# Optimization experiments

Hardware: AMD Instinct MI355X
Metric: run time of the kernel (lower is better)

## Reference

```python
import jax, jax.numpy as jnp
import numpy as np

N = 20000   # nodes
E = 320000  # edges
H = 128     # hidden_dim
L = 4       # num_layers
OUT = 64    # output_dim
XD = 16     # node_input_dim


def setup_inputs() -> dict:
    key = jax.random.key(0)
    ks = jax.random.split(key, 32)

    def w(k, shape):
        fan_in = shape[-2] if len(shape) >= 2 else shape[-1]
        return (jax.random.normal(k, shape, jnp.float32) / np.sqrt(fan_in)).astype(jnp.float32)

    inp = {
        'y': jax.random.normal(ks[0], (N, 6), jnp.float32),
        'x': jax.random.normal(ks[1], (N, XD), jnp.float32),
        'edge_attr': jax.random.normal(ks[2], (E, 8), jnp.float32),
        'edge_index': jax.random.randint(ks[3], (2, E), 0, N),
        'W_node': w(ks[4], (XD, H)),        'b_node': jnp.zeros((H,), jnp.float32),
        'W_eemb': w(ks[5], (5, H - 3)),     'b_eemb': jnp.zeros((H - 3,), jnp.float32),
        'W_msg': w(ks[6], (L, 3 * H + 1, H)), 'b_msg': jnp.zeros((L, H), jnp.float32),
        'W_upd': w(ks[7], (L, 2 * H, H)),     'b_upd': jnp.zeros((L, H), jnp.float32),
        'ln_g': jnp.ones((L, H), jnp.float32), 'ln_b': jnp.zeros((L, H), jnp.float32),
        'W_eu': w(ks[8], (L, 3 * H, H)),      'b_eu': jnp.zeros((L, H), jnp.float32),
        'W_out': w(ks[9], (H, OUT)),          'b_out': jnp.zeros((OUT,), jnp.float32),
        'Wh1': w(ks[10], (OUT, OUT // 2)),    'bh1': jnp.zeros((OUT // 2,), jnp.float32),
        'Wh2': w(ks[11], (OUT // 2, 1)),      'bh2': jnp.zeros((1,), jnp.float32),
    }
    return inp


def _drift(y, x, edge_attr, W_node, b_node, W_eemb, b_eemb, W_msg, b_msg,
           W_upd, b_upd, ln_g, ln_b, W_eu, b_eu, W_out, b_out,
           Wh1, bh1, Wh2, bh2, edge_index):
    src, dst = edge_index[0], edge_index[1]
    q, p = jnp.split(y, 2, axis=-1)  # each [N,3]

    def potential(q):
        pos = q
        h = x @ W_node + b_node                                    # [N,H]
        e = jnp.concatenate([edge_attr[:, :3],
                             edge_attr[:, 3:] @ W_eemb + b_eemb], -1)  # [E,H]
        for l in range(L):
            rel = pos[dst] - pos[src]                              # [E,3]
            dist = jnp.sqrt(jnp.sum(rel * rel, -1, keepdims=True) + 1e-8)
            m_in = jnp.concatenate([h[src], h[dst], e, dist], -1)  # [E,3H+1]
            m = jax.nn.silu(m_in @ W_msg[l] + b_msg[l])            # [E,H]
            agg = jax.ops.segment_sum(m, dst, num_segments=N)      # [N,H]
            u = jnp.concatenate([h, agg], -1) @ W_upd[l] + b_upd[l]
            mu = jnp.mean(u, -1, keepdims=True)
            var = jnp.var(u, -1, keepdims=True)
            u = (u - mu) / jnp.sqrt(var + 1e-5) * ln_g[l] + ln_b[l]
            h = h + jax.nn.silu(u)
            e = e + jax.nn.silu(jnp.concatenate([h[src], h[dst], e], -1) @ W_eu[l] + b_eu[l])
        f = h @ W_out + b_out                                      # [N,OUT]
        v = jax.nn.silu(f @ Wh1 + bh1) @ Wh2 + bh2                 # [N,1]
        return jnp.sum(v)

    grad_q = jax.grad(potential)(q)      # dH/dq
    # dH/dp = p (kinetic 0.5*sum(p*p)); drift = (dH/dp, -dH/dq)
    return jnp.concatenate([p, -grad_q], axis=-1)


def reference(y, x, edge_attr, edge_index, W_node, b_node, W_eemb, b_eemb,
              W_msg, b_msg, W_upd, b_upd, ln_g, ln_b, W_eu, b_eu,
              W_out, b_out, Wh1, bh1, Wh2, bh2):
    return _drift(y, x, edge_attr, W_node, b_node, W_eemb, b_eemb, W_msg, b_msg,
                  W_upd, b_upd, ln_g, ln_b, W_eu, b_eu, W_out, b_out,
                  Wh1, bh1, Wh2, bh2, edge_index)
```

## Files before the change

### kernel.cpp

```cpp
#include <hip/hip_runtime.h>
#include <hip/hip_bf16.h>

#define NN 20000
#define NE 320000
#define H  128
#define NL 4

typedef unsigned int uint;
typedef unsigned short u16;
typedef short s8v __attribute__((ext_vector_type(8)));
typedef float fx4 __attribute__((ext_vector_type(4)));

static constexpr size_t NNH = (size_t)NN*H;
static constexpr size_t NEH = (size_t)NE*H;

static constexpr size_t OFF_H5    = 0;
static constexpr size_t OFF_UPRE  = OFF_H5    + 5*NNH*2;
static constexpr size_t OFF_LNST  = OFF_UPRE  + 4*NNH*2;
static constexpr size_t OFF_T     = OFF_LNST  + (size_t)4*NN*2*4;
static constexpr size_t OFF_E     = OFF_T     + 4*NNH*2;
static constexpr size_t OFF_DE    = OFF_E     + NEH*2;
static constexpr size_t OFF_AGG   = OFF_DE    + NEH*2;
static constexpr size_t OFF_DH    = OFF_AGG   + NNH*4;
static constexpr size_t OFF_DIST  = OFF_DH    + NNH*4;
static constexpr size_t OFF_DDIST = OFF_DIST  + (size_t)NE*4;
static constexpr size_t OFF_DPOS  = OFF_DDIST + (size_t)NE*4;
static constexpr size_t OFF_WMT   = OFF_DPOS  + (size_t)NN*3*4;
static constexpr size_t OFF_WET   = OFF_WMT   + (size_t)NL*128*388*4;
static constexpr size_t OFF_WUT   = OFF_WET   + (size_t)NL*128*384*4;
static constexpr size_t OFF_PD    = OFF_WUT   + (size_t)NL*128*256*4;
static constexpr size_t OFF_PS    = OFF_PD    + (size_t)NE*4;
static constexpr size_t OFF_CURD  = OFF_PS    + (size_t)NE*4;
static constexpr size_t OFF_CURS  = OFF_CURD  + (size_t)NN*4;
static constexpr size_t OFF_WMP   = OFF_CURS  + (size_t)NN*4;
static constexpr size_t OFF_WEP   = OFF_WMP   + (size_t)NL*49152*2;
static constexpr size_t OFF_WMTP  = OFF_WEP   + (size_t)NL*49152*2;
static constexpr size_t OFF_WETP  = OFF_WMTP  + (size_t)NL*49152*2;
static constexpr size_t WS_NEED   = OFF_WETP  + (size_t)NL*49152*2;

__device__ __forceinline__ float sigm(float x){ return 1.f/(1.f+__expf(-x)); }
__device__ __forceinline__ float siluf(float x){ return x*sigm(x); }
__device__ __forceinline__ float dsilu(float x){ float s=sigm(x); return s*(1.f + x*(1.f-s)); }
__device__ __forceinline__ u16 f2bf(float x){
  uint u = __float_as_uint(x);
  uint r = (u + 0x7fffu + ((u>>16)&1u)) >> 16;
  return (u16)r;
}
__device__ __forceinline__ float bf2f(u16 v){ return __uint_as_float(((uint)v)<<16); }
__device__ __forceinline__ uint pack2(float a, float b){ return (uint)f2bf(a) | ((uint)f2bf(b)<<16); }
__device__ __forceinline__ void ld_bf8(const u16* p, float* v){
  uint4 q = *(const uint4*)p;
  v[0]=__uint_as_float(q.x<<16); v[1]=__uint_as_float(q.x&0xffff0000u);
  v[2]=__uint_as_float(q.y<<16); v[3]=__uint_as_float(q.y&0xffff0000u);
  v[4]=__uint_as_float(q.z<<16); v[5]=__uint_as_float(q.z&0xffff0000u);
  v[6]=__uint_as_float(q.w<<16); v[7]=__uint_as_float(q.w&0xffff0000u);
}
__device__ __forceinline__ void st_bf8(u16* p, const float* v){
  uint4 o;
  o.x = pack2(v[0],v[1]); o.y = pack2(v[2],v[3]);
  o.z = pack2(v[4],v[5]); o.w = pack2(v[6],v[7]);
  *(uint4*)p = o;
}

__device__ __forceinline__ float2 blockSum2_128(float a, float b, float* sb){
  #pragma unroll
  for (int off=32; off>0; off>>=1){ a += __shfl_down(a, off); b += __shfl_down(b, off); }
  int t = threadIdx.x;
  if ((t&63)==0){ sb[(t>>6)*2+0]=a; sb[(t>>6)*2+1]=b; }
  __syncthreads();
  float2 r; r.x = sb[0]+sb[2]; r.y = sb[1]+sb[3];
  __syncthreads();
  return r;
}

__device__ __forceinline__ void seg_walk136(const u16* Cst, const int* keys, float* buf, int t){
  int c = t & 127, half = t >> 7;
  int i0 = half*64, i1 = i0 + 64;
  float acc = 0.f; int k = keys[i0];
  #pragma unroll 4
  for (int i=i0; i<i1; i++){
    int ki = keys[i];
    if (ki != k){ atomicAdd(&buf[(size_t)k*H + c], acc); acc = 0.f; k = ki; }
    acc += bf2f(Cst[(size_t)i*136 + c]);
  }
  atomicAdd(&buf[(size_t)k*H + c], acc);
}

__global__ void diag_k(float* out, float v){ out[0] = v; }

__global__ void hist_k(const int* __restrict__ ei, int* __restrict__ curs, int* __restrict__ curd){
  int e = blockIdx.x*256 + threadIdx.x;
  if (e >= NE) return;
  atomicAdd(&curs[ei[e]], 1);
  atomicAdd(&curd[ei[NE+e]], 1);
}

__global__ __launch_bounds__(256) void scan_k(int* __restrict__ curd, int* __restrict__ curs){
  __shared__ int ps[256];
  const int t = threadIdx.x;
  const int CH = (NN + 255)/256;
  for (int a=0; a<2; a++){
    int* p = a ? curs : curd;
    int lo = t*CH, hi = lo+CH < NN ? lo+CH : NN;
    int sum = 0;
    for (int i=lo; i<hi; i++) sum += p[i];
    ps[t] = sum;
    __syncthreads();
    #pragma unroll
    for (int off=1; off<256; off<<=1){
      int v = (t>=off) ? ps[t-off] : 0;
      __syncthreads();
      ps[t] += v;
      __syncthreads();
    }
    int run = (t==0) ? 0 : ps[t-1];
    for (int i=lo; i<hi; i++){ int v = p[i]; p[i] = run; run += v; }
    __syncthreads();
  }
}

__global__ void fill_k(const int* __restrict__ ei, int* __restrict__ curs, int* __restrict__ curd,
                       int* __restrict__ perm_s, int* __restrict__ perm_d){
  int e = blockIdx.x*256 + threadIdx.x;
  if (e >= NE) return;
  perm_s[atomicAdd(&curs[ei[e]], 1)] = e;
  perm_d[atomicAdd(&curd[ei[NE+e]], 1)] = e;
}

__global__ void transpose_w(const float* __restrict__ Wm, const float* __restrict__ We,
                            const float* __restrict__ Wu,
                            float* __restrict__ WmT, float* __restrict__ WeT,
                            float* __restrict__ WuT){
  int idx = blockIdx.x*blockDim.x + threadIdx.x;
  int stride = gridDim.x*blockDim.x;
  for (int i=idx; i<NL*128*388; i+=stride){
    int l = i/(128*388), r = i - l*128*388, k = r/388, j = r - k*388;
    WmT[i] = (j<385) ? Wm[((size_t)l*385 + j)*H + k] : 0.f;
  }
  for (int i=idx; i<NL*128*384; i+=stride){
    int l = i/(128*384), r = i - l*128*384, k = r/384, j = r - k*384;
    WeT[i] = We[((size_t)l*384 + j)*H + k];
  }
  for (int i=idx; i<NL*128*256; i+=stride){
    int l = i/(128*256), r = i - l*128*256, k = r/256, j = r - k*256;
    WuT[i] = Wu[((size_t)l*256 + j)*H + k];
  }
}

__global__ __launch_bounds__(64) void pack_k(const float* __restrict__ src, u16* __restrict__ dst,
                      int KS, int NC, int ld, size_t sStride, size_t dStride){
  int b = blockIdx.x;
  int l = b/(KS*NC); int r = b - l*KS*NC; int ks = r/NC; int ct = r - ks*NC;
  int lane = threadIdx.x;
  #pragma unroll
  for (int j=0;j<8;j++){
    int k = ks*32 + (lane>>4)*8 + j;
    int c = ct*16 + (lane&15);
    dst[l*dStride + ((size_t)(ks*NC+ct)*64 + lane)*8 + j] =
        f2bf(src[l*sStride + (size_t)k*ld + c]);
  }
}

__global__ __launch_bounds__(128) void node_emb(const float* __restrict__ x,
                                                const float* __restrict__ Wn,
                                                const float* __restrict__ bn,
                                                u16* __restrict__ h){
  __shared__ float xs[16];
  int n = blockIdx.x, c = threadIdx.x;
  if (c < 16) xs[c] = x[(size_t)n*16 + c];
  __syncthreads();
  float s = bn[c];
  #pragma unroll
  for (int k=0;k<16;k++) s = fmaf(xs[k], Wn[k*H + c], s);
  h[(size_t)n*H + c] = f2bf(s);
}

__global__ __launch_bounds__(256) void edge_emb(const float* __restrict__ ea,
                                                const float* __restrict__ We5,
                                                const float* __restrict__ be,
                                                u16* __restrict__ ebuf){
  int e = blockIdx.x*2 + (threadIdx.x>>7);
  int c = threadIdx.x & 127;
  const float* row = ea + (size_t)e*8;
  float v;
  if (c < 3) v = row[c];
  else {
    int j = c-3;
    float s = be[j];
    #pragma unroll
    for (int k=0;k<5;k++) s = fmaf(row[3+k], We5[k*125 + j], s);
    v = s;
  }
  ebuf[(size_t)e*H + c] = f2bf(v);
}

__global__ void rel_dist(const float* __restrict__ y, const int* __restrict__ ei,
                         float* __restrict__ dist){
  int e = blockIdx.x*256 + threadIdx.x;
  if (e >= NE) return;
  int s = ei[e], d = ei[NE+e];
  float rx = y[(size_t)d*6+0] - y[(size_t)s*6+0];
  float ry = y[(size_t)d*6+1] - y[(size_t)s*6+1];
  float rz = y[(size_t)d*6+2] - y[(size_t)s*6+2];
  dist[e] = sqrtf(rx*rx + ry*ry + rz*rz + 1e-8f);
}

#define PHASE1_MFMA(ACC)                                                          \
  _Pragma("unroll 1")                                                             \
  for (int s=0; s<12; s++){                                                       \
    s8v av0, av1;                                                                 \
    {                                                                             \
      int k = s*32 + l4*8;                                                        \
      int row0 = wid*32 + li, row1 = row0 + 16;                                   \
      const u16 *p0, *p1;                                                         \
      if (k < 128){ p0 = hb + (size_t)sidx[row0]*H + k;                           \
                    p1 = hb + (size_t)sidx[row1]*H + k; }                         \
      else if (k < 256){ p0 = hb + (size_t)didx[row0]*H + (k-128);                \
                         p1 = hb + (size_t)didx[row1]*H + (k-128); }              \
      else { p0 = eb + (size_t)eidl[row0]*H + (k-256);                            \
             p1 = eb + (size_t)eidl[row1]*H + (k-256); }                          \
      av0 = *(const s8v*)p0; av1 = *(const s8v*)p1;                               \
    }                                                                             \
    _Pragma("unroll")                                                             \
    for (int ct=0; ct<8; ct++){                                                   \
      s8v bv = *(const s8v*)&WP[((size_t)(s*8+ct)*64 + lane)*8];                  \
      ACC[0][ct] = __builtin_amdgcn_mfma_f32_16x16x32_bf16(av0, bv, ACC[0][ct], 0,0,0); \
      ACC[1][ct] = __builtin_amdgcn_mfma_f32_16x16x32_bf16(av1, bv, ACC[1][ct], 0,0,0); \
    }                                                                             \
  }

template<int MODE>
__global__ __launch_bounds__(256) void efwd(
    const u16* __restrict__ hb, u16* __restrict__ eb,
    const float* __restrict__ dist, const int* __restrict__ ei,
    const int* __restrict__ perm,
    const float* __restrict__ Wf, const float* __restrict__ bias,
    const u16* __restrict__ WP,
    float* __restrict__ agg, float* __restrict__ Tf)
{
  __shared__ __align__(16) u16 Als[128*136];
  __shared__ int eidl[128], sidx[128], didx[128];
  const int t = threadIdx.x;
  const int e0 = blockIdx.x * 128;
  if (t < 128){
    int eid = perm ? perm[e0+t] : (e0+t);
    eidl[t] = eid; sidx[t] = ei[eid]; didx[t] = ei[NE+eid];
  }
  __syncthreads();
  const int lane = t&63, wid = t>>6, l4 = lane>>4, li = lane&15;

  fx4 acc[2][8];
  #pragma unroll
  for (int i=0;i<2;i++){
    #pragma unroll
    for (int j=0;j<8;j++) acc[i][j] = (fx4){0.f,0.f,0.f,0.f};
  }
  PHASE1_MFMA(acc)

  float dv[2][4];
  if (MODE==0){
    #pragma unroll
    for (int rt=0;rt<2;rt++){
      #pragma unroll
      for (int reg=0;reg<4;reg++) dv[rt][reg] = dist[eidl[wid*32+rt*16+l4*4+reg]];
    }
  }
  #pragma unroll
  for (int ct=0; ct<8; ct++){
    int c = ct*16 + li;
    float bi = bias[c];
    float wd = (MODE==0) ? Wf[(size_t)384*H + c] : 0.f;
    #pragma unroll
    for (int rt=0;rt<2;rt++){
      #pragma unroll
      for (int reg=0;reg<4;reg++)
        acc[rt][ct][reg] += bi + ((MODE==0) ? dv[rt][reg]*wd : 0.f);
    }
  }

  if (MODE==0){
    __syncthreads();
    #pragma unroll
    for (int rt=0;rt<2;rt++){
      #pragma unroll
      for (int reg=0;reg<4;reg++){
        int brow = wid*32+rt*16+l4*4+reg;
        #pragma unroll
        for (int ct=0;ct<8;ct++)
          Als[(size_t)brow*136 + ct*16+li] = f2bf(siluf(acc[rt][ct][reg]));
      }
    }
    __syncthreads();
    seg_walk136(Als, didx, agg, t);
    __syncthreads();
    #pragma unroll
    for (int rt=0;rt<2;rt++){
      #pragma unroll
      for (int reg=0;reg<4;reg++){
        int brow = wid*32+rt*16+l4*4+reg;
        #pragma unroll
        for (int ct=0;ct<8;ct++)
          Als[(size_t)brow*136 + ct*16+li] = f2bf(dsilu(acc[rt][ct][reg]));
      }
    }
    __syncthreads();
    seg_walk136(Als, didx, Tf, t);
  } else {
    __syncthreads();
    #pragma unroll
    for (int rt=0;rt<2;rt++){
      #pragma unroll
      for (int reg=0;reg<4;reg++){
        int brow = wid*32+rt*16+l4*4+reg;
        #pragma unroll
        for (int ct=0;ct<8;ct++)
          Als[(size_t)brow*136 + ct*16+li] = f2bf(siluf(acc[rt][ct][reg]));
      }
    }
    __syncthreads();
    int row = t>>1, coff = (t&1)*64;
    u16* dst = eb + (size_t)eidl[row]*H + coff;
    #pragma unroll
    for (int i=0;i<8;i++){
      float a[8], b[8];
      ld_bf8(&Als[(size_t)row*136 + coff + i*8], a);
      ld_bf8(&dst[i*8], b);
      #pragma unroll
      for (int j=0;j<8;j++) b[j] += a[j];
      st_bf8(&dst[i*8], b);
    }
  }
}

template<int MODE>
__global__ __launch_bounds__(256) void ebwd(
    const u16* __restrict__ hb, const u16* __restrict__ eb,
    const float* __restrict__ dist, const int* __restrict__ ei,
    const int* __restrict__ perm,
    const float* __restrict__ Wf, const float* __restrict__ bias,
    const float* __restrict__ mulf, const float* __restrict__ WTf,
    const u16* __restrict__ WP, const u16* __restrict__ WTP,
    float* __restrict__ dh, u16* __restrict__ de, float* __restrict__ ddist)
{
  __shared__ __align__(16) u16 Als[128*136];
  __shared__ int eidl[128], sidx[128], didx[128];
  const int t = threadIdx.x;
  const int e0 = blockIdx.x * 128;
  if (t < 128){
    int eid = perm[e0+t];
    eidl[t] = eid; sidx[t] = ei[eid]; didx[t] = ei[NE+eid];
  }
  __syncthreads();
  const int lane = t&63, wid = t>>6, l4 = lane>>4, li = lane&15;

  fx4 acc[2][8];
  #pragma unroll
  for (int i=0;i<2;i++){
    #pragma unroll
    for (int j=0;j<8;j++) acc[i][j] = (fx4){0.f,0.f,0.f,0.f};
  }
  PHASE1_MFMA(acc)

  float dv[2][4];
  if (MODE==0){
    #pragma unroll
    for (int rt=0;rt<2;rt++){
      #pragma unroll
      for (int reg=0;reg<4;reg++) dv[rt][reg] = dist[eidl[wid*32+rt*16+l4*4+reg]];
    }
  }
  #pragma unroll
  for (int ct=0; ct<8; ct++){
    int c = ct*16 + li;
    float bi = bias[c];
    float wd = (MODE==0) ? Wf[(size_t)384*H + c] : 0.f;
    #pragma unroll
    for (int rt=0;rt<2;rt++){
      #pragma unroll
      for (int reg=0;reg<4;reg++)
        acc[rt][ct][reg] += bi + ((MODE==0) ? dv[rt][reg]*wd : 0.f);
    }
  }

  if (MODE==1){
    {
      int row = t>>1, coff = (t&1)*64;
      const u16* src = de + (size_t)eidl[row]*H + coff;
      #pragma unroll
      for (int i=0;i<8;i++)
        *(uint4*)&Als[(size_t)row*136 + coff + i*8] = *(const uint4*)&src[i*8];
    }
    __syncthreads();
  }
  #pragma unroll
  for (int rt=0;rt<2;rt++){
    #pragma unroll
    for (int reg=0;reg<4;reg++){
      int brow = wid*32+rt*16+l4*4+reg;
      #pragma unroll
      for (int ct=0;ct<8;ct++){
        int c = ct*16+li;
        float m;
        if (MODE==0) m = mulf[(size_t)didx[brow]*H + c];
        else         m = bf2f(Als[(size_t)brow*136 + c]);
        acc[rt][ct][reg] = m * dsilu(acc[rt][ct][reg]);
      }
    }
  }

  if (MODE==0){
    float wdT[8];
    #pragma unroll
    for (int ct=0;ct<8;ct++) wdT[ct] = WTf[(size_t)(ct*16+li)*388 + 384];
    #pragma unroll
    for (int rt=0;rt<2;rt++){
      #pragma unroll
      for (int reg=0;reg<4;reg++){
        float pd = 0.f;
        #pragma unroll
        for (int ct=0;ct<8;ct++) pd = fmaf(acc[rt][ct][reg], wdT[ct], pd);
        pd += __shfl_xor(pd, 1);
        pd += __shfl_xor(pd, 2);
        pd += __shfl_xor(pd, 4);
        pd += __shfl_xor(pd, 8);
        if (li == 0) ddist[eidl[wid*32+rt*16+l4*4+reg]] += pd;
      }
    }
  }

  __syncthreads();
  #pragma unroll
  for (int rt=0;rt<2;rt++){
    #pragma unroll
    for (int reg=0;reg<4;reg++){
      int brow = wid*32+rt*16+l4*4+reg;
      #pragma unroll
      for (int ct=0;ct<8;ct++)
        Als[(size_t)brow*136 + ct*16+li] = f2bf(acc[rt][ct][reg]);
    }
  }
  __syncthreads();

  s8v afr[2][4];
  #pragma unroll
  for (int rt=0;rt<2;rt++){
    int row = wid*32 + rt*16 + li;
    #pragma unroll
    for (int ks=0;ks<4;ks++)
      afr[rt][ks] = *(const s8v*)&Als[(size_t)row*136 + ks*32 + l4*8];
  }

  const int njc = (MODE==0) ? 2 : 3;
  const int jcl[3] = {2, (MODE==0)?0:1, 0};
  #pragma unroll 1
  for (int ji=0; ji<njc; ji++){
    const int jc = jcl[ji];
    #pragma unroll
    for (int i=0;i<2;i++){
      #pragma unroll
      for (int j=0;j<8;j++) acc[i][j] = (fx4){0.f,0.f,0.f,0.f};
    }
    #pragma unroll
    for (int ks=0;ks<4;ks++){
      #pragma unroll
      for (int ct=0;ct<8;ct++){
        s8v bv = *(const s8v*)&WTP[((size_t)(ks*24 + jc*8 + ct)*64 + lane)*8];
        acc[0][ct] = __builtin_amdgcn_mfma_f32_16x16x32_bf16(afr[0][ks], bv, acc[0][ct], 0,0,0);
        acc[1][ct] = __builtin_amdgcn_mfma_f32_16x16x32_bf16(afr[1][ks], bv, acc[1][ct], 0,0,0);
      }
    }
    if (jc == 1){
      #pragma unroll
      for (int rt=0;rt<2;rt++){
        #pragma unroll
        for (int reg=0;reg<4;reg++){
          int dn = didx[wid*32+rt*16+l4*4+reg];
          #pragma unroll
          for (int ct=0;ct<8;ct++)
            atomicAdd(&dh[(size_t)dn*H + ct*16+li], acc[rt][ct][reg]);
        }
      }
    } else {
      __syncthreads();
      #pragma unroll
      for (int rt=0;rt<2;rt++){
        #pragma unroll
        for (int reg=0;reg<4;reg++){
          int brow = wid*32+rt*16+l4*4+reg;
          #pragma unroll
          for (int ct=0;ct<8;ct++)
            Als[(size_t)brow*136 + ct*16+li] = f2bf(acc[rt][ct][reg]);
        }
      }
      __syncthreads();
      if (jc == 2){
        int row = t>>1, coff = (t&1)*64;
        u16* dst = de + (size_t)eidl[row]*H + coff;
        #pragma unroll
        for (int i=0;i<8;i++){
          float a[8], b[8];
          ld_bf8(&Als[(size_t)row*136 + coff + i*8], a);
          ld_bf8(&dst[i*8], b);
          #pragma unroll
          for (int j=0;j<8;j++) b[j] += a[j];
          st_bf8(&dst[i*8], b);
        }
      } else {
        seg_walk136(Als, sidx, dh, t);
      }
    }
  }
}

__global__ __launch_bounds__(128) void upd_fwd(
    const u16* __restrict__ hin, const float* __restrict__ agg,
    const float* __restrict__ Wu, const float* __restrict__ bu,
    const float* __restrict__ g, const float* __restrict__ bln,
    u16* __restrict__ upre, float* __restrict__ lnst, u16* __restrict__ hout,
    u16* __restrict__ T, float* __restrict__ Tf)
{
  __shared__ float ha[8][256];
  __shared__ float sb[4];
  const int n0 = blockIdx.x*8, c = threadIdx.x;
  #pragma unroll
  for (int n=0;n<8;n++){
    ha[n][c]     = bf2f(hin[(size_t)(n0+n)*H + c]);
    ha[n][128+c] = agg[(size_t)(n0+n)*H + c];
  }
  __syncthreads();
  float s[8];
  float bv = bu[c];
  #pragma unroll
  for (int n=0;n<8;n++) s[n] = bv;
  #pragma unroll 2
  for (int k=0;k<256;k++){
    float w = Wu[(size_t)k*H + c];
    #pragma unroll
    for (int n=0;n<8;n++) s[n] = fmaf(ha[n][k], w, s[n]);
  }
  float gc = g[c], bc = bln[c];
  #pragma unroll 1
  for (int n=0;n<8;n++){
    int nn = n0+n;
    upre[(size_t)nn*H + c] = f2bf(s[n]);
    float2 ms = blockSum2_128(s[n], s[n]*s[n], sb);
    float mu = ms.x*(1.f/128.f);
    float var = ms.y*(1.f/128.f) - mu*mu;
    float rstd = rsqrtf(var + 1e-5f);
    if (c == 0){ lnst[(size_t)nn*2+0] = mu; lnst[(size_t)nn*2+1] = rstd; }
    float uh = (s[n] - mu)*rstd;
    float un = uh*gc + bc;
    hout[(size_t)nn*H + c] = f2bf(ha[n][c] + siluf(un));
    size_t idx = (size_t)nn*H + c;
    T[idx] = f2bf(Tf[idx]);
    Tf[idx] = 0.f;
  }
}

__global__ __launch_bounds__(128) void final_fused(
    const u16* __restrict__ h, const float* __restrict__ Wo, const float* __restrict__ bo,
    const float* __restrict__ Wh1, const float* __restrict__ bh1v,
    const float* __restrict__ Wh2, float* __restrict__ dh)
{
  __shared__ float sh[8][128], sf[8][64], sdz[8][32], sdf[8][64];
  const int n0 = blockIdx.x*8, c = threadIdx.x;
  #pragma unroll
  for (int n=0;n<8;n++) sh[n][c] = bf2f(h[(size_t)(n0+n)*H + c]);
  __syncthreads();
  if (c < 64){
    float s[8]; float bv = bo[c];
    #pragma unroll
    for (int n=0;n<8;n++) s[n] = bv;
    #pragma unroll 2
    for (int k=0;k<128;k++){
      float w = Wo[(size_t)k*64 + c];
      #pragma unroll
      for (int n=0;n<8;n++) s[n] = fmaf(sh[n][k], w, s[n]);
    }
    #pragma unroll
    for (int n=0;n<8;n++) sf[n][c] = s[n];
  }
  __syncthreads();
  if (c < 32){
    float s[8]; float bv = bh1v[c];
    #pragma unroll
    for (int n=0;n<8;n++) s[n] = bv;
    #pragma unroll 2
    for (int j=0;j<64;j++){
      float w = Wh1[(size_t)j*32 + c];
      #pragma unroll
      for (int n=0;n<8;n++) s[n] = fmaf(sf[n][j], w, s[n]);
    }
    float w2 = Wh2[c];
    #pragma unroll
    for (int n=0;n<8;n++) sdz[n][c] = w2*dsilu(s[n]);
  }
  __syncthreads();
  if (c < 64){
    float s[8];
    #pragma unroll
    for (int n=0;n<8;n++) s[n] = 0.f;
    #pragma unroll 2
    for (int k=0;k<32;k++){
      float w = Wh1[(size_t)c*32 + k];
      #pragma unroll
      for (int n=0;n<8;n++) s[n] = fmaf(sdz[n][k], w, s[n]);
    }
    #pragma unroll
    for (int n=0;n<8;n++) sdf[n][c] = s[n];
  }
  __syncthreads();
  {
    float s[8];
    #pragma unroll
    for (int n=0;n<8;n++) s[n] = 0.f;
    #pragma unroll 2
    for (int j=0;j<64;j++){
      float w = Wo[(size_t)c*64 + j];
      #pragma unroll
      for (int n=0;n<8;n++) s[n] = fmaf(sdf[n][j], w, s[n]);
    }
    #pragma unroll
    for (int n=0;n<8;n++) dh[(size_t)(n0+n)*H + c] = s[n];
  }
}

__global__ __launch_bounds__(128) void upd_bwd(
    float* __restrict__ dh, float* __restrict__ dagg,
    const u16* __restrict__ upre, const float* __restrict__ lnst,
    const float* __restrict__ WuT, const u16* __restrict__ T,
    const float* __restrict__ WmT,
    const float* __restrict__ g, const float* __restrict__ bln)
{
  __shared__ float sh[8][128];
  __shared__ float qs[8][128];
  __shared__ float sb[4];
  const int n0 = blockIdx.x*8, c = threadIdx.x;
  const float gc = g[c], bc = bln[c];
  float dhv[8];
  #pragma unroll 1
  for (int n=0;n<8;n++){
    int nn = n0+n;
    float up   = bf2f(upre[(size_t)nn*H + c]);
    float mu   = lnst[(size_t)nn*2+0];
    float rstd = lnst[(size_t)nn*2+1];
    float uh = (up - mu)*rstd;
    float un = uh*gc + bc;
    dhv[n] = dh[(size_t)nn*H + c];
    float dun = dhv[n] * dsilu(un);
    float duh = dun * gc;
    float2 m12 = blockSum2_128(duh, duh*uh, sb);
    sh[n][c] = (duh - m12.x*(1.f/128.f) - uh*(m12.y*(1.f/128.f)))*rstd;
  }
  __syncthreads();
  float s0[8], s1[8];
  #pragma unroll
  for (int n=0;n<8;n++){ s0[n]=0.f; s1[n]=0.f; }
  #pragma unroll 2
  for (int k=0;k<128;k++){
    float w0 = WuT[(size_t)k*256 + c];
    float w1 = WuT[(size_t)k*256 + 128 + c];
    #pragma unroll
    for (int n=0;n<8;n++){
      float d = sh[n][k];
      s0[n] = fmaf(d, w0, s0[n]);
      s1[n] = fmaf(d, w1, s1[n]);
    }
  }
  #pragma unroll
  for (int n=0;n<8;n++){
    int nn = n0+n;
    dagg[(size_t)nn*H + c] = s1[n];
    qs[n][c] = s1[n] * bf2f(T[(size_t)nn*H + c]);
  }
  __syncthreads();
  float a2[8];
  #pragma unroll
  for (int n=0;n<8;n++) a2[n] = 0.f;
  #pragma unroll 2
  for (int k=0;k<128;k++){
    float w = WmT[(size_t)k*388 + 128 + c];
    #pragma unroll
    for (int n=0;n<8;n++) a2[n] = fmaf(qs[n][k], w, a2[n]);
  }
  #pragma unroll
  for (int n=0;n<8;n++) dh[(size_t)(n0+n)*H + c] = dhv[n] + s0[n] + a2[n];
}

__global__ void rel_bwd(const float* __restrict__ y, const float* __restrict__ dist,
                        const float* __restrict__ ddist, const int* __restrict__ ei,
                        float* __restrict__ dpos){
  int e = blockIdx.x*256 + threadIdx.x;
  if (e >= NE) return;
  int s = ei[e], d = ei[NE+e];
  float gsc = ddist[e]/dist[e];
  #pragma unroll
  for (int i=0;i<3;i++){
    float dr = gsc*(y[(size_t)d*6+i] - y[(size_t)s*6+i]);
    atomicAdd(&dpos[(size_t)d*3+i],  dr);
    atomicAdd(&dpos[(size_t)s*3+i], -dr);
  }
}

__global__ void out_k(const float* __restrict__ y, const float* __restrict__ dpos,
                      float* __restrict__ out){
  int n = blockIdx.x*256 + threadIdx.x;
  if (n >= NN) return;
  #pragma unroll
  for (int i=0;i<3;i++) out[(size_t)n*6+i]   =  y[(size_t)n*6+3+i];
  #pragma unroll
  for (int i=0;i<3;i++) out[(size_t)n*6+3+i] = -dpos[(size_t)n*3+i];
}

extern "C" void kernel_launch(void* const* d_in, const int* in_sizes, int n_in,
                              void* d_out, int out_size, void* d_ws, size_t ws_size,
                              hipStream_t stream)
{
  const float* y   = (const float*)d_in[0];
  const float* x   = (const float*)d_in[1];
  const float* ea  = (const float*)d_in[2];
  const int*   ei  = (const int*)d_in[3];
  const float* Wn  = (const float*)d_in[4];
  const float* bn  = (const float*)d_in[5];
  const float* We5 = (const float*)d_in[6];
  const float* be5 = (const float*)d_in[7];
  const float* Wm  = (const float*)d_in[8];
  const float* bm  = (const float*)d_in[9];
  const float* Wu  = (const float*)d_in[10];
  const float* bu  = (const float*)d_in[11];
  const float* lg  = (const float*)d_in[12];
  const float* lb  = (const float*)d_in[13];
  const float* We  = (const float*)d_in[14];
  const float* beu = (const float*)d_in[15];
  const float* Wo  = (const float*)d_in[16];
  const float* bo  = (const float*)d_in[17];
  const float* Wh1 = (const float*)d_in[18];
  const float* bh1v= (const float*)d_in[19];
  const float* Wh2 = (const float*)d_in[20];
  float* out = (float*)d_out;

  if (ws_size < WS_NEED){
    diag_k<<<1, 1, 0, stream>>>(out, 4000.f + (float)(ws_size >> 20));
    return;
  }

  char* ws = (char*)d_ws;
  u16*   h5    = (u16*)  (ws + OFF_H5);
  u16*   upre  = (u16*)  (ws + OFF_UPRE);
  float* lnst  = (float*)(ws + OFF_LNST);
  u16*   T     = (u16*)  (ws + OFF_T);
  u16*   eb    = (u16*)  (ws + OFF_E);
  u16*   de    = (u16*)  (ws + OFF_DE);
  float* aggd  = (float*)(ws + OFF_AGG);
  float* dh    = (float*)(ws + OFF_DH);
  float* dist  = (float*)(ws + OFF_DIST);
  float* ddist = (float*)(ws + OFF_DDIST);
  float* dpos  = (float*)(ws + OFF_DPOS);
  float* WmT   = (float*)(ws + OFF_WMT);
  float* WeT   = (float*)(ws + OFF_WET);
  float* WuT   = (float*)(ws + OFF_WUT);
  int*   perm_d= (int*)  (ws + OFF_PD);
  int*   perm_s= (int*)  (ws + OFF_PS);
  int*   curd  = (int*)  (ws + OFF_CURD);
  int*   curs  = (int*)  (ws + OFF_CURS);
  u16*   WmP   = (u16*)  (ws + OFF_WMP);
  u16*   WeP   = (u16*)  (ws + OFF_WEP);
  u16*   WmTP  = (u16*)  (ws + OFF_WMTP);
  u16*   WeTP  = (u16*)  (ws + OFF_WETP);

  hipMemsetAsync(ddist, 0, (size_t)NE*4, stream);
  hipMemsetAsync(dpos,  0, (size_t)NN*3*4, stream);
  hipMemsetAsync(de,    0, NEH*2, stream);
  hipMemsetAsync(dh,    0, NNH*4, stream);
  hipMemsetAsync(curd,  0, (size_t)NN*4, stream);
  hipMemsetAsync(curs,  0, (size_t)NN*4, stream);

  transpose_w<<<512, 256, 0, stream>>>(Wm, We, Wu, WmT, WeT, WuT);
  pack_k<<<NL*12*8, 64, 0, stream>>>(Wm,  WmP,  12, 8,  128, (size_t)385*128, 49152);
  pack_k<<<NL*12*8, 64, 0, stream>>>(We,  WeP,  12, 8,  128, (size_t)384*128, 49152);
  pack_k<<<NL*4*24, 64, 0, stream>>>(WmT, WmTP, 4,  24, 388, (size_t)128*388, 49152);
  pack_k<<<NL*4*24, 64, 0, stream>>>(WeT, WeTP, 4,  24, 384, (size_t)128*384, 49152);

  node_emb<<<NN, 128, 0, stream>>>(x, Wn, bn, h5);
  edge_emb<<<NE/2, 256, 0, stream>>>(ea, We5, be5, eb);
  rel_dist<<<NE/256, 256, 0, stream>>>(y, ei, dist);

  hist_k<<<NE/256, 256, 0, stream>>>(ei, curs, curd);
  scan_k<<<1, 256, 0, stream>>>(curd, curs);
  fill_k<<<NE/256, 256, 0, stream>>>(ei, curs, curd, perm_s, perm_d);

  for (int l=0; l<NL; l++){
    hipMemsetAsync(aggd, 0, NNH*4, stream);
    efwd<0><<<NE/128, 256, 0, stream>>>(h5 + l*NNH, eb, dist, ei, perm_d,
        Wm + (size_t)l*385*H, bm + (size_t)l*H, WmP + (size_t)l*49152, aggd, dh);
    upd_fwd<<<NN/8, 128, 0, stream>>>(h5 + l*NNH, aggd,
        Wu + (size_t)l*256*H, bu + (size_t)l*H,
        lg + (size_t)l*H, lb + (size_t)l*H,
        upre + l*NNH, lnst + (size_t)l*NN*2, h5 + (l+1)*NNH,
        T + l*NNH, dh);
    if (l < NL-1){
      efwd<1><<<NE/128, 256, 0, stream>>>(h5 + (l+1)*NNH, eb, nullptr, ei, nullptr,
          We + (size_t)l*384*H, beu + (size_t)l*H, WeP + (size_t)l*49152, nullptr, nullptr);
    }
  }

  final_fused<<<NN/8, 128, 0, stream>>>(h5 + (size_t)NL*NNH, Wo, bo, Wh1, bh1v, Wh2, dh);

  for (int l=NL-1; l>=0; l--){
    if (l < NL-1){
      edge_emb<<<NE/2, 256, 0, stream>>>(ea, We5, be5, eb);
      for (int k=0; k<l; k++){
        efwd<1><<<NE/128, 256, 0, stream>>>(h5 + (k+1)*NNH, eb, nullptr, ei, nullptr,
            We + (size_t)k*384*H, beu + (size_t)k*H, WeP + (size_t)k*49152, nullptr, nullptr);
      }
      ebwd<1><<<NE/128, 256, 0, stream>>>(h5 + (l+1)*NNH, eb, nullptr, ei, perm_s,
          We + (size_t)l*384*H, beu + (size_t)l*H, nullptr, nullptr,
          WeP + (size_t)l*49152, WeTP + (size_t)l*49152, dh, de, nullptr);
    }
    upd_bwd<<<NN/8, 128, 0, stream>>>(dh, aggd, upre + l*NNH, lnst + (size_t)l*NN*2,
        WuT + (size_t)l*128*256, T + l*NNH, WmT + (size_t)l*128*388,
        lg + (size_t)l*H, lb + (size_t)l*H);
    ebwd<0><<<NE/128, 256, 0, stream>>>(h5 + l*NNH, eb, dist, ei, perm_s,
        Wm + (size_t)l*385*H, bm + (size_t)l*H, aggd, WmT + (size_t)l*128*388,
        WmP + (size_t)l*49152, WmTP + (size_t)l*49152, dh, de, ddist);
  }

  rel_bwd<<<NE/256, 256, 0, stream>>>(y, dist, ddist, ei, dpos);
  out_k<<<(NN+255)/256, 256, 0, stream>>>(y, dpos, out);
}
```

Measured before the change: 3.780 ms.

## Store per-edge buffers in source-sorted order to make edge accesses contiguous

All per-edge buffers (edge features, dist, edge grads) are now stored in source-sorted order: edge_emb and rel_dist write through perm_s, and perm_d is remapped into that order via an inverse permutation. Backward edge kernels then read edge rows contiguously instead of gathering through a permutation, and forward efwd<1> also walks edges in source order, which may improve h locality. The cost is an extra remap kernel and an extra indirection when loading original edge indices. The ddist buffer is temporarily reused to hold the inverse permutation before being zeroed.

```diff
diff --git a/kernel.cpp b/kernel.cpp
--- a/kernel.cpp
+++ b/kernel.cpp
@@ -120,11 +120,19 @@
 }
 
 __global__ void fill_k(const int* __restrict__ ei, int* __restrict__ curs, int* __restrict__ curd,
-                       int* __restrict__ perm_s, int* __restrict__ perm_d){
+                       int* __restrict__ perm_s, int* __restrict__ perm_d, int* __restrict__ inv){
   int e = blockIdx.x*256 + threadIdx.x;
   if (e >= NE) return;
-  perm_s[atomicAdd(&curs[ei[e]], 1)] = e;
+  int ns = atomicAdd(&curs[ei[e]], 1);
+  perm_s[ns] = e;
+  inv[e] = ns;
   perm_d[atomicAdd(&curd[ei[NE+e]], 1)] = e;
+}
+
+__global__ void remap_k(int* __restrict__ perm_d, const int* __restrict__ inv){
+  int j = blockIdx.x*256 + threadIdx.x;
+  if (j >= NE) return;
+  perm_d[j] = inv[perm_d[j]];
 }
 
 __global__ void transpose_w(const float* __restrict__ Wm, const float* __restrict__ We,
@@ -178,10 +186,11 @@
 __global__ __launch_bounds__(256) void edge_emb(const float* __restrict__ ea,
                                                 const float* __restrict__ We5,
                                                 const float* __restrict__ be,
+                                                const int* __restrict__ perm_s,
                                                 u16* __restrict__ ebuf){
   int e = blockIdx.x*2 + (threadIdx.x>>7);
   int c = threadIdx.x & 127;
-  const float* row = ea + (size_t)e*8;
+  const float* row = ea + (size_t)perm_s[e]*8;
   float v;
   if (c < 3) v = row[c];
   else {
@@ -195,10 +204,11 @@
 }
 
 __global__ void rel_dist(const float* __restrict__ y, const int* __restrict__ ei,
-                         float* __restrict__ dist){
+                         const int* __restrict__ perm_s, float* __restrict__ dist){
   int e = blockIdx.x*256 + threadIdx.x;
   if (e >= NE) return;
-  int s = ei[e], d = ei[NE+e];
+  int o = perm_s[e];
+  int s = ei[o], d = ei[NE+o];
   float rx = y[(size_t)d*6+0] - y[(size_t)s*6+0];
   float ry = y[(size_t)d*6+1] - y[(size_t)s*6+1];
   float rz = y[(size_t)d*6+2] - y[(size_t)s*6+2];
@@ -229,11 +239,18 @@
     }                                                                             \
   }
 
+#define LOAD_IDX(PORDER)                                                          \
+  if (t < 128){                                                                   \
+    int nid = (PORDER) ? (PORDER)[e0+t] : (e0+t);                                 \
+    int orig = perm_s[nid];                                                       \
+    eidl[t] = nid; sidx[t] = ei[orig]; didx[t] = ei[NE+orig];                     \
+  }
+
 template<int MODE>
 __global__ __launch_bounds__(256) void efwd(
     const u16* __restrict__ hb, u16* __restrict__ eb,
     const float* __restrict__ dist, const int* __restrict__ ei,
-    const int* __restrict__ perm,
+    const int* __restrict__ porder, const int* __restrict__ perm_s,
     const float* __restrict__ Wf, const float* __restrict__ bias,
     const u16* __restrict__ WP,
     float* __restrict__ agg, float* __restrict__ Tf)
@@ -242,10 +259,7 @@
   __shared__ int eidl[128], sidx[128], didx[128];
   const int t = threadIdx.x;
   const int e0 = blockIdx.x * 128;
-  if (t < 128){
-    int eid = perm ? perm[e0+t] : (e0+t);
-    eidl[t] = eid; sidx[t] = ei[eid]; didx[t] = ei[NE+eid];
-  }
+  LOAD_IDX(porder)
   __syncthreads();
   const int lane = t&63, wid = t>>6, l4 = lane>>4, li = lane&15;
 
@@ -336,7 +350,7 @@
 __global__ __launch_bounds__(256) void ebwd(
     const u16* __restrict__ hb, const u16* __restrict__ eb,
     const float* __restrict__ dist, const int* __restrict__ ei,
-    const int* __restrict__ perm,
+    const int* __restrict__ perm_s,
     const float* __restrict__ Wf, const float* __restrict__ bias,
     const float* __restrict__ mulf, const float* __restrict__ WTf,
     const u16* __restrict__ WP, const u16* __restrict__ WTP,
@@ -346,10 +360,7 @@
   __shared__ int eidl[128], sidx[128], didx[128];
   const int t = threadIdx.x;
   const int e0 = blockIdx.x * 128;
-  if (t < 128){
-    int eid = perm[e0+t];
-    eidl[t] = eid; sidx[t] = ei[eid]; didx[t] = ei[NE+eid];
-  }
+  LOAD_IDX((const int*)nullptr)
   __syncthreads();
   const int lane = t&63, wid = t>>6, l4 = lane>>4, li = lane&15;
 
@@ -689,10 +700,11 @@
 
 __global__ void rel_bwd(const float* __restrict__ y, const float* __restrict__ dist,
                         const float* __restrict__ ddist, const int* __restrict__ ei,
-                        float* __restrict__ dpos){
+                        const int* __restrict__ perm_s, float* __restrict__ dpos){
   int e = blockIdx.x*256 + threadIdx.x;
   if (e >= NE) return;
-  int s = ei[e], d = ei[NE+e];
+  int o = perm_s[e];
+  int s = ei[o], d = ei[NE+o];
   float gsc = ddist[e]/dist[e];
   #pragma unroll
   for (int i=0;i<3;i++){
@@ -768,7 +780,6 @@
   u16*   WmTP  = (u16*)  (ws + OFF_WMTP);
   u16*   WeTP  = (u16*)  (ws + OFF_WETP);
 
-  hipMemsetAsync(ddist, 0, (size_t)NE*4, stream);
   hipMemsetAsync(dpos,  0, (size_t)NN*3*4, stream);
   hipMemsetAsync(de,    0, NEH*2, stream);
   hipMemsetAsync(dh,    0, NNH*4, stream);
@@ -782,16 +793,19 @@
   pack_k<<<NL*4*24, 64, 0, stream>>>(WeT, WeTP, 4,  24, 384, (size_t)128*384, 49152);
 
   node_emb<<<NN, 128, 0, stream>>>(x, Wn, bn, h5);
-  edge_emb<<<NE/2, 256, 0, stream>>>(ea, We5, be5, eb);
-  rel_dist<<<NE/256, 256, 0, stream>>>(y, ei, dist);
 
   hist_k<<<NE/256, 256, 0, stream>>>(ei, curs, curd);
   scan_k<<<1, 256, 0, stream>>>(curd, curs);
-  fill_k<<<NE/256, 256, 0, stream>>>(ei, curs, curd, perm_s, perm_d);
+  fill_k<<<NE/256, 256, 0, stream>>>(ei, curs, curd, perm_s, perm_d, (int*)ddist);
+  remap_k<<<NE/256, 256, 0, stream>>>(perm_d, (const int*)ddist);
+  hipMemsetAsync(ddist, 0, (size_t)NE*4, stream);
+
+  edge_emb<<<NE/2, 256, 0, stream>>>(ea, We5, be5, perm_s, eb);
+  rel_dist<<<NE/256, 256, 0, stream>>>(y, ei, perm_s, dist);
 
   for (int l=0; l<NL; l++){
     hipMemsetAsync(aggd, 0, NNH*4, stream);
-    efwd<0><<<NE/128, 256, 0, stream>>>(h5 + l*NNH, eb, dist, ei, perm_d,
+    efwd<0><<<NE/128, 256, 0, stream>>>(h5 + l*NNH, eb, dist, ei, perm_d, perm_s,
         Wm + (size_t)l*385*H, bm + (size_t)l*H, WmP + (size_t)l*49152, aggd, dh);
     upd_fwd<<<NN/8, 128, 0, stream>>>(h5 + l*NNH, aggd,
         Wu + (size_t)l*256*H, bu + (size_t)l*H,
@@ -799,7 +813,7 @@
         upre + l*NNH, lnst + (size_t)l*NN*2, h5 + (l+1)*NNH,
         T + l*NNH, dh);
     if (l < NL-1){
-      efwd<1><<<NE/128, 256, 0, stream>>>(h5 + (l+1)*NNH, eb, nullptr, ei, nullptr,
+      efwd<1><<<NE/128, 256, 0, stream>>>(h5 + (l+1)*NNH, eb, nullptr, ei, nullptr, perm_s,
           We + (size_t)l*384*H, beu + (size_t)l*H, WeP + (size_t)l*49152, nullptr, nullptr);
     }
   }
@@ -808,9 +822,9 @@
 
   for (int l=NL-1; l>=0; l--){
     if (l < NL-1){
-      edge_emb<<<NE/2, 256, 0, stream>>>(ea, We5, be5, eb);
+      edge_emb<<<NE/2, 256, 0, stream>>>(ea, We5, be5, perm_s, eb);
       for (int k=0; k<l; k++){
-        efwd<1><<<NE/128, 256, 0, stream>>>(h5 + (k+1)*NNH, eb, nullptr, ei, nullptr,
+        efwd<1><<<NE/128, 256, 0, stream>>>(h5 + (k+1)*NNH, eb, nullptr, ei, nullptr, perm_s,
             We + (size_t)k*384*H, beu + (size_t)k*H, WeP + (size_t)k*49152, nullptr, nullptr);
       }
       ebwd<1><<<NE/128, 256, 0, stream>>>(h5 + (l+1)*NNH, eb, nullptr, ei, perm_s,
@@ -825,6 +839,6 @@
         WmP + (size_t)l*49152, WmTP + (size_t)l*49152, dh, de, ddist);
   }
 
-  rel_bwd<<<NE/256, 256, 0, stream>>>(y, dist, ddist, ei, dpos);
+  rel_bwd<<<NE/256, 256, 0, stream>>>(y, dist, ddist, ei, perm_s, dpos);
   out_k<<<(NN+255)/256, 256, 0, stream>>>(y, dpos, out);
 }
```

Result: no change. 3.802 ms (+0.6%).
